# Optimization experiments

Measured on AMD Instinct MI355X. Metric: run time of the kernel, lower is better.

## Reference

```python
import jax, jax.numpy as jnp
import numpy as np

B, L_IN, D = 4, 4096, 1024
R_MIN, R_MAX = 0.9, 0.999


def setup_inputs() -> dict:
    key = jax.random.key(0)
    k0, k1, k2 = jax.random.split(key, 3)
    inputs = jax.random.normal(k0, (B, L_IN, D), jnp.float32)
    Wi = jax.random.normal(k1, (2 * D, D), jnp.float32) / np.sqrt(D)
    bi = jnp.zeros((2 * D,), jnp.float32)
    Wo = jax.random.normal(k2, (D, 2 * D), jnp.float32) / np.sqrt(2 * D)
    bo = jnp.zeros((D,), jnp.float32)
    # LRU stable-ring initialization, exactly as in the torch module
    rng = np.random.default_rng(0)
    u1 = rng.random(D)
    u2 = rng.random(D)
    v_log = np.log(-0.5 * np.log(u1 * (R_MAX ** 2 - R_MIN ** 2) + R_MIN ** 2))
    theta_log = np.log(u2 * np.pi * 2)
    gamma_log = np.log(np.sqrt(1.0 - np.exp(-np.exp(v_log)) ** 2))
    params_log = jnp.asarray(np.stack([v_log, theta_log, gamma_log]), jnp.float32)
    return {"inputs": inputs, "Wi": Wi, "bi": bi, "Wo": Wo, "bo": bo,
            "params_log": params_log}


def _lru_forward(inputs, Wi, bi, Wo, bo, params_log):
    b, l_in, d = inputs.shape
    u = inputs @ Wi.T + bi                      # [B, L, 2D]
    v, theta, gamma = jnp.exp(params_log)       # each [D]
    # torch.view_as_complex: interleaved (real, imag) pairs along last dim
    uc = u.reshape(b, l_in, d, 2)
    x = jax.lax.complex(uc[..., 0], uc[..., 1])  # [B, L, D] complex64
    log2_L = int(np.ceil(np.log2(l_in)))
    L = 2 ** log2_L
    x = jnp.pad(x, ((0, 0), (0, L - l_in), (0, 0)))
    # Blelloch-style log-depth scan: x_t = lambda * x_{t-1} + u_t,
    # lambda = exp(-v + i*theta)
    for i in range(1, log2_L + 1):
        blk = 2 ** i
        xb = x.reshape(b * L // blk, blk, d)
        x1, x2 = xb[:, : blk // 2], xb[:, blk // 2:]
        pos = jnp.arange(1, blk // 2 + 1, dtype=jnp.float32)  # [blk/2]
        lambs = jnp.exp(jax.lax.complex(-pos[:, None] * v,
                                        pos[:, None] * theta))  # [blk/2, D]
        x2 = x2 + lambs * x1[:, -1:]
        x = jnp.concatenate([x1, x2], axis=1).reshape(b, L, d)
    x = x[:, :l_in] * gamma.astype(x.dtype)     # normalize, drop padding
    xr = jnp.concatenate([x.real, x.imag], axis=-1)  # [B, L, 2D]
    out = xr @ Wo.T + bo
    return jax.nn.relu(out)


def reference(inputs, Wi, bi, Wo, bo, params_log):
    return _lru_forward(inputs, Wi, bi, Wo, bo, params_log)
```

## Files before the change

kernel.cpp:

```cpp
#include <hip/hip_runtime.h>

#define BB 4
#define LL 4096
#define DD 1024
#define SS 128
#define TT 32

typedef __attribute__((ext_vector_type(4))) float  floatx4;
typedef __attribute__((ext_vector_type(8))) short  shortx8;
typedef __attribute__((ext_vector_type(8))) unsigned short ushortx8;

static __device__ __forceinline__ unsigned short f2bf(float f) {
    unsigned int u = __float_as_uint(f);
    u += 0x7fffu + ((u >> 16) & 1u);
    return (unsigned short)(u >> 16);
}
static __device__ __forceinline__ float bf2f(unsigned short h) {
    return __uint_as_float(((unsigned int)h) << 16);
}

#define NIN4 (BB * LL * DD / 4)
#define NWI4 (2 * DD * DD / 4)
#define NWO8 (DD * DD / 4)
__global__ void cast_all_kernel(const float4* __restrict__ s_in, ushort4* __restrict__ d_inb,
                                const float4* __restrict__ s_wi, ushort4* __restrict__ d_wib,
                                const float* __restrict__ s_wo, unsigned short* __restrict__ d_wob) {
    int i = blockIdx.x * blockDim.x + threadIdx.x;
    if (i < NIN4 + NWI4) {
        const float4* s; ushort4* d; int j;
        if (i < NIN4) { s = s_in; d = d_inb; j = i; }
        else          { s = s_wi; d = d_wib; j = i - NIN4; }
        float4 v = s[j];
        ushort4 o;
        o.x = f2bf(v.x); o.y = f2bf(v.y); o.z = f2bf(v.z); o.w = f2bf(v.w);
        d[j] = o;
    } else {
        int j = i - NIN4 - NWI4;
        int n  = j >> 8;
        int d0 = (j & 255) * 4;
        const float* rowp = s_wo + (size_t)n * (2 * DD);
        float4 re = *(const float4*)(rowp + d0);
        float4 im = *(const float4*)(rowp + DD + d0);
        ushortx8 o;
        o[0] = f2bf(re.x); o[1] = f2bf(im.x);
        o[2] = f2bf(re.y); o[3] = f2bf(im.y);
        o[4] = f2bf(re.z); o[5] = f2bf(im.z);
        o[6] = f2bf(re.w); o[7] = f2bf(im.w);
        *(ushortx8*)(d_wob + (size_t)n * (2 * DD) + 2 * d0) = o;
    }
}

template<int K, int NT, int EPI>
__global__ __launch_bounds__(512, 2)
void gemm256(const unsigned short* __restrict__ A,
             const unsigned short* __restrict__ B,
             const float* __restrict__ bias,
             void* __restrict__ Cp) {
    constexpr int N   = NT * 256;
    constexpr int NKT = K / 64;
    __shared__ __align__(16) short As[2][256 * 64];
    __shared__ __align__(16) short Bs[2][256 * 64];

    const int tid = threadIdx.x;
    const int blk = blockIdx.x;
    const int xcd = blk & 7;
    const int i2  = blk >> 3;
    const int tileM = ((i2 / NT) * 8 + xcd) * 256;
    const int tileN = (i2 % NT) * 256;

    const int lane   = tid & 63;
    const int wave   = tid >> 6;
    const int wave_m = wave >> 2;
    const int wave_n = wave & 3;
    const int r16    = lane & 15;
    const int quad   = lane >> 4;
    const int slotx  = r16 & 7;
    const int wmRow  = wave_m * 64 + r16;
    const int wnRow  = wave_n * 32 + r16;

    const int srow = tid >> 3;
    const int scol = ((tid & 7) ^ (srow & 7)) * 8;
    const int ldsChunkBase = (tid & ~63) * 8;
    const size_t aOff = (size_t)(tileM + srow) * K + scol;
    const size_t bOff = (size_t)(tileN + srow) * K + scol;

    floatx4 acc[8][4] = {};
    shortx8 af[4][2], bf0v[2][2], bf1v[2][2];

#define GLL(SRC, DST) __builtin_amdgcn_global_load_lds( \
        (const __attribute__((address_space(1))) void*)(SRC), \
        (__attribute__((address_space(3))) void*)(DST), 16, 0, 0)
#define STAGE_A(BUF, H, KT) do { \
    GLL(A + aOff + (size_t)((H) * 128) * K + (KT) * 64,      &As[BUF][(H) * 8192 + ldsChunkBase]); \
    GLL(A + aOff + (size_t)((H) * 128 + 64) * K + (KT) * 64, &As[BUF][(H) * 8192 + 4096 + ldsChunkBase]); \
} while (0)
#define STAGE_B(BUF, H, KT) do { \
    GLL(B + bOff + (size_t)((H) * 128) * K + (KT) * 64,      &Bs[BUF][(H) * 8192 + ldsChunkBase]); \
    GLL(B + bOff + (size_t)((H) * 128 + 64) * K + (KT) * 64, &Bs[BUF][(H) * 8192 + 4096 + ldsChunkBase]); \
} while (0)
#define LOAD_A(BUF, MH) do { \
    _Pragma("unroll") for (int il = 0; il < 4; ++il) \
    _Pragma("unroll") for (int kk = 0; kk < 2; ++kk) \
        af[il][kk] = *(const shortx8*)&As[BUF][((MH) * 128 + wmRow + il * 16) * 64 + ((kk * 4 + quad) ^ slotx) * 8]; \
} while (0)
#define LOAD_B(BUF, NH, DST) do { \
    _Pragma("unroll") for (int jl = 0; jl < 2; ++jl) \
    _Pragma("unroll") for (int kk = 0; kk < 2; ++kk) \
        DST[jl][kk] = *(const shortx8*)&Bs[BUF][((NH) * 128 + wnRow + jl * 16) * 64 + ((kk * 4 + quad) ^ slotx) * 8]; \
} while (0)
#define MFMAQ(MH, NH, BF) do { \
    __builtin_amdgcn_s_setprio(1); \
    _Pragma("unroll") for (int kk = 0; kk < 2; ++kk) \
    _Pragma("unroll") for (int il = 0; il < 4; ++il) \
    _Pragma("unroll") for (int jl = 0; jl < 2; ++jl) \
        acc[(MH) * 4 + il][(NH) * 2 + jl] = __builtin_amdgcn_mfma_f32_16x16x32_bf16( \
            af[il][kk], BF[jl][kk], acc[(MH) * 4 + il][(NH) * 2 + jl], 0, 0, 0); \
    __builtin_amdgcn_s_setprio(0); \
} while (0)
#define BAR()  __builtin_amdgcn_s_barrier()
#define LGKM0() asm volatile("s_waitcnt lgkmcnt(0)" ::: "memory")

    STAGE_A(0, 0, 0);
    STAGE_B(0, 0, 0);
    STAGE_B(0, 1, 0);
    STAGE_A(0, 1, 0);
    STAGE_A(1, 0, 1);
    STAGE_B(1, 1, 1);
    STAGE_A(1, 1, 1);
    asm volatile("s_waitcnt vmcnt(6)" ::: "memory");
    BAR();
    LOAD_A(0, 0);
    LOAD_B(0, 0, bf0v);

#pragma unroll 2
    for (int t = 0; t < NKT; ++t) {
        const int cb = t & 1;
        const int t1 = (t + 1 < NKT) ? t + 1 : NKT - 1;
        const int t2 = (t + 2 < NKT) ? t + 2 : NKT - 1;
        BAR();
        LGKM0();
        STAGE_B(cb ^ 1, 0, t1);
        MFMAQ(0, 0, bf0v);
        LOAD_B(cb, 1, bf1v);
        BAR();
        LGKM0();
        STAGE_A(cb, 0, t2);
        MFMAQ(0, 1, bf1v);
        LOAD_A(cb, 1);
        BAR();
        LGKM0();
        STAGE_B(cb, 1, t2);
        MFMAQ(1, 0, bf0v);
        asm volatile("s_waitcnt vmcnt(4)" ::: "memory");
        BAR();
        STAGE_A(cb, 1, t2);
        MFMAQ(1, 1, bf1v);
        LOAD_A(cb ^ 1, 0);
        LOAD_B(cb ^ 1, 0, bf0v);
    }
    asm volatile("s_waitcnt vmcnt(0) lgkmcnt(0)" ::: "memory");

#pragma unroll
    for (int i = 0; i < 8; ++i) {
        const int row0 = tileM + (i >> 2) * 128 + wave_m * 64 + (i & 3) * 16 + quad * 4;
#pragma unroll
        for (int j = 0; j < 4; ++j) {
            const int col = tileN + (j >> 1) * 128 + wave_n * 32 + (j & 1) * 16 + r16;
            const float bv = bias[col];
#pragma unroll
            for (int r = 0; r < 4; ++r) {
                float v = acc[i][j][r] + bv;
                if (EPI == 0) {
                    ((unsigned short*)Cp)[(size_t)(row0 + r) * N + col] = f2bf(v);
                } else {
                    ((float*)Cp)[(size_t)(row0 + r) * N + col] = fmaxf(v, 0.0f);
                }
            }
        }
    }
#undef GLL
#undef STAGE_A
#undef STAGE_B
#undef LOAD_A
#undef LOAD_B
#undef MFMAQ
#undef BAR
#undef LGKM0
}

__global__ __launch_bounds__(256)
void scanA(const unsigned short* __restrict__ u,
           const float* __restrict__ plog,
           float2* __restrict__ Eend) {
    const int d = blockIdx.x * 256 + threadIdx.x;
    const int c = blockIdx.y, b = blockIdx.z;
    const float v  = expf(plog[d]);
    const float th = expf(plog[DD + d]);
    const float a  = expf(-v);
    const float lr = a * cosf(th), li = a * sinf(th);
    float zr = 0.f, zi = 0.f;
    const unsigned short* up = u + (size_t)(b * LL + c * TT) * (2 * DD) + 2 * d;
#pragma unroll 8
    for (int tl = 0; tl < TT; ++tl) {
        unsigned int pr = *(const unsigned int*)up;
        float xr = bf2f((unsigned short)(pr & 0xffffu));
        float xi = bf2f((unsigned short)(pr >> 16));
        float t = lr * zr - li * zi + xr;
        zi = lr * zi + li * zr + xi;
        zr = t;
        up += 2 * DD;
    }
    Eend[(size_t)c * (BB * DD) + b * DD + d] = make_float2(zr, zi);
}

__global__ __launch_bounds__(64)
void scanB(const float* __restrict__ plog, float2* __restrict__ E) {
    const int i = blockIdx.x * 64 + threadIdx.x;
    const int d = i & (DD - 1);
    const float v  = expf(plog[d]);
    const float th = expf(plog[DD + d]);
    const float aT = expf(-(float)TT * v);
    const float Lr = aT * cosf((float)TT * th), Li = aT * sinf((float)TT * th);
    float yr = 0.f, yi = 0.f;
    float2* p = E + i;
#pragma unroll 16
    for (int c = 0; c < SS; ++c) {
        float2 e = *p;
        *p = make_float2(yr, yi);
        float t = Lr * yr - Li * yi + e.x;
        yi = Lr * yi + Li * yr + e.y;
        yr = t;
        p += BB * DD;
    }
}

__global__ __launch_bounds__(256)
void scanC(const unsigned short* __restrict__ u,
           const float* __restrict__ plog,
           const float2* __restrict__ Carry,
           unsigned short* __restrict__ xr) {
    const int d = blockIdx.x * 256 + threadIdx.x;
    const int c = blockIdx.y, b = blockIdx.z;
    const float v  = expf(plog[d]);
    const float th = expf(plog[DD + d]);
    const float g  = expf(plog[2 * DD + d]);
    const float a  = expf(-v);
    const float lr = a * cosf(th), li = a * sinf(th);
    const float2 cy = Carry[(size_t)c * (BB * DD) + b * DD + d];
    float yr = cy.x, yi = cy.y;
    const unsigned short* up = u + (size_t)(b * LL + c * TT) * (2 * DD) + 2 * d;
    unsigned short* xp = xr + (size_t)(b * LL + c * TT) * (2 * DD) + 2 * d;
#pragma unroll 8
    for (int tl = 0; tl < TT; ++tl) {
        unsigned int pr = *(const unsigned int*)up;
        float xrv = bf2f((unsigned short)(pr & 0xffffu));
        float xiv = bf2f((unsigned short)(pr >> 16));
        float t = lr * yr - li * yi + xrv;
        yi = lr * yi + li * yr + xiv;
        yr = t;
        *(unsigned int*)xp = (unsigned int)f2bf(g * yr) |
                             ((unsigned int)f2bf(g * yi) << 16);
        up += 2 * DD;
        xp += 2 * DD;
    }
}

extern "C" void kernel_launch(void* const* d_in, const int* in_sizes, int n_in,
                              void* d_out, int out_size, void* d_ws, size_t ws_size,
                              hipStream_t stream) {
    const float* inputs = (const float*)d_in[0];
    const float* Wi     = (const float*)d_in[1];
    const float* bi     = (const float*)d_in[2];
    const float* Wo     = (const float*)d_in[3];
    const float* bo     = (const float*)d_in[4];
    const float* plog   = (const float*)d_in[5];
    float* out = (float*)d_out;

    const size_t M = (size_t)BB * LL;
    unsigned short* u_bf  = (unsigned short*)d_ws;
    unsigned short* xr_bf = u_bf  + M * 2 * DD;
    unsigned short* in_bf = xr_bf + M * 2 * DD;
    unsigned short* Wi_bf = in_bf + M * DD;
    unsigned short* Wo_bf = Wi_bf + (size_t)2 * DD * DD;
    float2* Eend = (float2*)in_bf;

    {
        int total = NIN4 + NWI4 + NWO8;
        cast_all_kernel<<<total / 256, 256, 0, stream>>>(
            (const float4*)inputs, (ushort4*)in_bf,
            (const float4*)Wi,     (ushort4*)Wi_bf,
            Wo,                    Wo_bf);
    }

    gemm256<DD, 8, 0><<<(M / 256) * 8, 512, 0, stream>>>(
        in_bf, Wi_bf, bi, (void*)u_bf);

    scanA<<<dim3(DD / 256, SS, BB), 256, 0, stream>>>(u_bf, plog, Eend);
    scanB<<<(BB * DD) / 64, 64, 0, stream>>>(plog, Eend);
    scanC<<<dim3(DD / 256, SS, BB), 256, 0, stream>>>(u_bf, plog, Eend, xr_bf);

    gemm256<2 * DD, 4, 1><<<(M / 256) * 4, 512, 0, stream>>>(
        xr_bf, Wo_bf, bo, (void*)out);
}
```

Before: 301.8 us.

## Fuse three scan phases into one cooperative kernel with grid syncs

Measured after the change: 300.7 us. About the same (-0.4%).

```diff
diff --git a/kernel.cpp b/kernel.cpp
--- a/kernel.cpp
+++ b/kernel.cpp
@@ -1,4 +1,5 @@
 #include <hip/hip_runtime.h>
+#include <hip/hip_cooperative_groups.h>
 
 #define BB 4
 #define LL 4096
@@ -188,6 +189,82 @@
 #undef LGKM0
 }
 
+__global__ __launch_bounds__(256, 8)
+void scan_fused(const unsigned short* __restrict__ u,
+                const float* __restrict__ plog,
+                float2* __restrict__ E,
+                unsigned short* __restrict__ xr) {
+    const int d = blockIdx.x * 256 + threadIdx.x;
+    const int c = blockIdx.y, b = blockIdx.z;
+
+    unsigned int w[TT];
+    {
+        const unsigned short* up = u + (size_t)(b * LL + c * TT) * (2 * DD) + 2 * d;
+#pragma unroll
+        for (int tl = 0; tl < TT; ++tl) { w[tl] = *(const unsigned int*)up; up += 2 * DD; }
+    }
+    {
+        const float v  = expf(plog[d]);
+        const float th = expf(plog[DD + d]);
+        const float a  = expf(-v);
+        const float lr = a * cosf(th), li = a * sinf(th);
+        float zr = 0.f, zi = 0.f;
+#pragma unroll
+        for (int tl = 0; tl < TT; ++tl) {
+            float xv = bf2f((unsigned short)(w[tl] & 0xffffu));
+            float yv = bf2f((unsigned short)(w[tl] >> 16));
+            float t = lr * zr - li * zi + xv;
+            zi = lr * zi + li * zr + yv;
+            zr = t;
+        }
+        E[(size_t)c * (BB * DD) + b * DD + d] = make_float2(zr, zi);
+    }
+    __threadfence();
+    cooperative_groups::this_grid().sync();
+
+    if (c == 0) {
+        const float v  = expf(plog[d]);
+        const float th = expf(plog[DD + d]);
+        const float aT = expf(-(float)TT * v);
+        const float Lr = aT * cosf((float)TT * th), Li = aT * sinf((float)TT * th);
+        float yr = 0.f, yi = 0.f;
+        float2* p = E + (size_t)b * DD + d;
+#pragma unroll 8
+        for (int cc = 0; cc < SS; ++cc) {
+            float2 e = *p;
+            *p = make_float2(yr, yi);
+            float t = Lr * yr - Li * yi + e.x;
+            yi = Lr * yi + Li * yr + e.y;
+            yr = t;
+            p += BB * DD;
+        }
+    }
+    __threadfence();
+    cooperative_groups::this_grid().sync();
+
+    {
+        const float v  = expf(plog[d]);
+        const float th = expf(plog[DD + d]);
+        const float g  = expf(plog[2 * DD + d]);
+        const float a  = expf(-v);
+        const float lr = a * cosf(th), li = a * sinf(th);
+        const float2 cy = E[(size_t)c * (BB * DD) + b * DD + d];
+        float yr = cy.x, yi = cy.y;
+        unsigned short* xp = xr + (size_t)(b * LL + c * TT) * (2 * DD) + 2 * d;
+#pragma unroll
+        for (int tl = 0; tl < TT; ++tl) {
+            float xv = bf2f((unsigned short)(w[tl] & 0xffffu));
+            float yv = bf2f((unsigned short)(w[tl] >> 16));
+            float t = lr * yr - li * yi + xv;
+            yi = lr * yi + li * yr + yv;
+            yr = t;
+            *(unsigned int*)xp = (unsigned int)f2bf(g * yr) |
+                                 ((unsigned int)f2bf(g * yi) << 16);
+            xp += 2 * DD;
+        }
+    }
+}
+
 __global__ __launch_bounds__(256)
 void scanA(const unsigned short* __restrict__ u,
            const float* __restrict__ plog,
@@ -213,9 +290,9 @@
     Eend[(size_t)c * (BB * DD) + b * DD + d] = make_float2(zr, zi);
 }
 
-__global__ __launch_bounds__(64)
+__global__ __launch_bounds__(256)
 void scanB(const float* __restrict__ plog, float2* __restrict__ E) {
-    const int i = blockIdx.x * 64 + threadIdx.x;
+    const int i = blockIdx.x * 256 + threadIdx.x;
     const int d = i & (DD - 1);
     const float v  = expf(plog[d]);
     const float th = expf(plog[DD + d]);
@@ -223,7 +300,7 @@
     const float Lr = aT * cosf((float)TT * th), Li = aT * sinf((float)TT * th);
     float yr = 0.f, yi = 0.f;
     float2* p = E + i;
-#pragma unroll 16
+#pragma unroll 8
     for (int c = 0; c < SS; ++c) {
         float2 e = *p;
         *p = make_float2(yr, yi);
@@ -295,9 +372,26 @@
     gemm256<DD, 8, 0><<<(M / 256) * 8, 512, 0, stream>>>(
         in_bf, Wi_bf, bi, (void*)u_bf);
 
-    scanA<<<dim3(DD / 256, SS, BB), 256, 0, stream>>>(u_bf, plog, Eend);
-    scanB<<<(BB * DD) / 64, 64, 0, stream>>>(plog, Eend);
-    scanC<<<dim3(DD / 256, SS, BB), 256, 0, stream>>>(u_bf, plog, Eend, xr_bf);
+    bool coop = false;
+    {
+        int nb = 0;
+        hipError_t qe = hipOccupancyMaxActiveBlocksPerMultiprocessor(&nb, scan_fused, 256, 0);
+        if (qe == hipSuccess && nb >= 8) {
+            const unsigned short* u_arg = u_bf;
+            const float* p_arg = plog;
+            float2* e_arg = Eend;
+            unsigned short* x_arg = xr_bf;
+            void* args[] = { (void*)&u_arg, (void*)&p_arg, (void*)&e_arg, (void*)&x_arg };
+            hipError_t le = hipLaunchCooperativeKernel(scan_fused,
+                dim3(DD / 256, SS, BB), dim3(256), args, 0, stream);
+            coop = (le == hipSuccess);
+        }
+    }
+    if (!coop) {
+        scanA<<<dim3(DD / 256, SS, BB), 256, 0, stream>>>(u_bf, plog, Eend);
+        scanB<<<(BB * DD) / 256, 256, 0, stream>>>(plog, Eend);
+        scanC<<<dim3(DD / 256, SS, BB), 256, 0, stream>>>(u_bf, plog, Eend, xr_bf);
+    }
 
     gemm256<2 * DD, 4, 1><<<(M / 256) * 4, 512, 0, stream>>>(
         xr_bf, Wo_bf, bo, (void*)out);
```
